# Kernel optimization log

Hardware: AMD Instinct MI355X
Metric: run time of the kernel (lower is better)

The kernel has to match this reference:

```python
import jax, jax.numpy as jnp
import numpy as np

N_NODES = 50000
N_EDGES = 600000
NODE_DIM = 128
EDGE_DIM = 128
HIDDEN = 256
OUT_DIM = 16
MAX_DEG = 10  # PyG MFConv default max_degree
N_GRAPHS = 256
N_MESSAGES = 2


def setup_inputs() -> dict:
    key = jax.random.key(0)
    ks = jax.random.split(key, 10)
    s = 0.05
    x = jax.random.normal(ks[0], (N_NODES, NODE_DIM), jnp.float32)
    edge_attr = jax.random.normal(ks[1], (N_EDGES, EDGE_DIM), jnp.float32)
    edge_index = jax.random.randint(ks[2], (2, N_EDGES), 0, N_NODES, jnp.int32)
    batch = jnp.sort(jax.random.randint(ks[3], (N_NODES,), 0, N_GRAPHS, jnp.int32))
    # MFConv params: lins (on aggregated neighbors, with bias), root_lins (no bias)
    W_lin = jax.random.normal(ks[4], (MAX_DEG + 1, NODE_DIM, NODE_DIM), jnp.float32) * s
    b_lin = jnp.zeros((MAX_DEG + 1, NODE_DIM), jnp.float32)
    W_root = jax.random.normal(ks[5], (MAX_DEG + 1, NODE_DIM, NODE_DIM), jnp.float32) * s
    # EdgeConv nn: Linear(2*edge_dim, edge_dim)
    W_edge = jax.random.normal(ks[6], (2 * EDGE_DIM, EDGE_DIM), jnp.float32) * s
    b_edge = jnp.zeros((EDGE_DIM,), jnp.float32)
    # readout MLP (n_hidden=1): Linear(2*node_dim, hidden), Linear(hidden, out)
    W0 = jax.random.normal(ks[7], (2 * NODE_DIM, HIDDEN), jnp.float32) * s
    b0 = jnp.zeros((HIDDEN,), jnp.float32)
    W1 = jax.random.normal(ks[8], (HIDDEN, OUT_DIM), jnp.float32) * s
    b1 = jnp.zeros((OUT_DIM,), jnp.float32)
    return {"x": x, "edge_attr": edge_attr, "edge_index": edge_index, "batch": batch,
            "W_lin": W_lin, "b_lin": b_lin, "W_root": W_root,
            "W_edge": W_edge, "b_edge": b_edge,
            "W0": W0, "b0": b0, "W1": W1, "b1": b1}


def _mfconv(x, row, col, deg, W_lin, b_lin, W_root):
    # h[i] = sum_{(j->i)} x[j]  (source_to_target flow: row=src, col=dst)
    h = jax.ops.segment_sum(x[row], col, num_segments=N_NODES)
    out = jnp.zeros_like(h)
    for d in range(MAX_DEG + 1):  # fixed small degree-bucket loop
        m = (deg == d).astype(x.dtype)[:, None]
        out = out + m * (h @ W_lin[d] + b_lin[d] + x @ W_root[d])
    return out


def _edgeconv(e, row, col, W, b):
    # message: nn([x_i, x_j - x_i]); aggr = max over incoming edges (empty -> 0)
    xi = e[col]
    msg = jnp.concatenate([xi, e[row] - xi], axis=-1) @ W + b
    out = jax.ops.segment_max(msg, col, num_segments=e.shape[0])
    return jnp.where(jnp.isfinite(out), out, jnp.zeros_like(out))


def reference(x, edge_attr, edge_index, batch, W_lin, b_lin, W_root, W_edge, b_edge, W0, b0, W1, b1):
    row, col = edge_index[0], edge_index[1]
    deg = jnp.clip(jax.ops.segment_sum(jnp.ones((N_EDGES,), jnp.int32), col,
                                       num_segments=N_NODES), 0, MAX_DEG)
    emb_node = x
    emb_edge = edge_attr
    for _ in range(N_MESSAGES):
        x = _mfconv(x, row, col, deg, W_lin, b_lin, W_root)
        emb_node = x
        x = jax.nn.relu(x)  # dropout p=0.0 in eval -> identity
        edge_attr = _edgeconv(edge_attr, row, col, W_edge, b_edge)
        emb_edge = edge_attr
        edge_attr = jax.nn.relu(edge_attr)
    # readout: gather-concat-scatter_add over edges, then global add pool
    out = jnp.concatenate([x[row], edge_attr[col]], axis=-1)  # [E, 2*node_dim]
    out = jax.ops.segment_sum(out, col, num_segments=N_NODES)  # [N, 2*node_dim]
    out = jax.ops.segment_sum(out, batch, num_segments=N_GRAPHS)  # [G, 2*node_dim]
    out = jax.nn.relu(out @ W0 + b0)
    out = jax.nn.relu(out @ W1 + b1)
    return out, emb_node, emb_edge
```

## Files before the change

### kernel.cpp

```cpp
#include <hip/hip_runtime.h>
#include <cfloat>

#define N_NODES 50000
#define N_EDGES 600000
#define DIM 128
#define N_GRAPHS 256
#define HIDDEN 256
#define OUT_DIM 16
#define MAX_DEG 10
#define MAX_TBL 1600
#define GEMM_GRID 1563
#define AGG_GRID 12500
#define EB 2344
#define NB 196
#define XCONV_B 6250
#define WF_B 176
#define WEF_B 16

typedef unsigned short u16;
typedef __attribute__((ext_vector_type(8))) short bf16x8;
typedef __attribute__((ext_vector_type(4))) float f32x4;

__device__ __forceinline__ float bf2f(u16 u) {
  union { unsigned u; float f; } c; c.u = ((unsigned)u) << 16; return c.f;
}
__device__ __forceinline__ u16 f2bf(float f) {
  union { float f; unsigned u; } c; c.f = f;
  return (u16)((c.u + 0x7FFFu + ((c.u >> 16) & 1u)) >> 16);
}
__device__ __forceinline__ float4 relu4(float4 v) {
  return make_float4(fmaxf(v.x, 0.f), fmaxf(v.y, 0.f), fmaxf(v.z, 0.f), fmaxf(v.w, 0.f));
}
__device__ __forceinline__ void fma4b(float4& a, float m, ushort4 v) {
  a.x = fmaf(m, bf2f(v.x), a.x); a.y = fmaf(m, bf2f(v.y), a.y);
  a.z = fmaf(m, bf2f(v.z), a.z); a.w = fmaf(m, bf2f(v.w), a.w);
}
__device__ __forceinline__ void max4b(float4& a, ushort4 v) {
  a.x = fmaxf(a.x, bf2f(v.x)); a.y = fmaxf(a.y, bf2f(v.y));
  a.z = fmaxf(a.z, bf2f(v.z)); a.w = fmaxf(a.w, bf2f(v.w));
}

__global__ __launch_bounds__(256) void kPrep(
    const float* __restrict__ x_in, u16* __restrict__ xb,
    const float* __restrict__ W_lin, const float* __restrict__ W_root,
    u16* __restrict__ Wfrag, const float* __restrict__ W_edge,
    u16* __restrict__ Wefrag, const int* __restrict__ col, int* __restrict__ deg) {
  int b = blockIdx.x, t = threadIdx.x;
  if (b < XCONV_B) {
    size_t i = ((size_t)b * 256 + t) * 4;
    float4 v = *(const float4*)(x_in + i);
    ushort4 o; o.x = f2bf(v.x); o.y = f2bf(v.y); o.z = f2bf(v.z); o.w = f2bf(v.w);
    *(ushort4*)(xb + i) = o;
  } else if (b < XCONV_B + WF_B) {
    int tid = (b - XCONV_B) * 256 + t;
    int lane = tid & 63, f = tid >> 6;
    int d = f >> 6, rem = f & 63, ks = rem >> 3, nt = rem & 7;
    u16* dst = Wfrag + ((size_t)f * 64 + lane) * 8;
    int n = nt * 16 + (lane & 15);
#pragma unroll
    for (int j = 0; j < 8; ++j) {
      int k = ks * 32 + (lane >> 4) * 8 + j;
      float v = (k < 128) ? W_lin[((size_t)d * 128 + k) * 128 + n]
                          : W_root[((size_t)d * 128 + (k - 128)) * 128 + n];
      dst[j] = f2bf(v);
    }
  } else if (b < XCONV_B + WF_B + WEF_B) {
    int tid = (b - XCONV_B - WF_B) * 256 + t;
    int lane = tid & 63, f = tid >> 6;
    int ks = f >> 4, nt = f & 15;
    u16* dst = Wefrag + ((size_t)f * 64 + lane) * 8;
    int n2 = nt * 16 + (lane & 15);
#pragma unroll
    for (int j = 0; j < 8; ++j) {
      int k = ks * 32 + (lane >> 4) * 8 + j;
      float v;
      if (n2 < 128) v = W_edge[(size_t)(128 + k) * 128 + n2];
      else { int n = n2 - 128; v = W_edge[(size_t)k * 128 + n] - W_edge[(size_t)(128 + k) * 128 + n]; }
      dst[j] = f2bf(v);
    }
  } else {
    int e = (b - XCONV_B - WF_B - WEF_B) * 256 + t;
    if (e < N_EDGES) atomicAdd(&deg[col[e]], 1);
  }
}

__global__ void k_setup(const int* __restrict__ deg, const int* __restrict__ batch,
                        int* __restrict__ rowptr, int* __restrict__ cursor,
                        int* __restrict__ bcur, int* __restrict__ tbl_d,
                        int* __restrict__ tbl_base, int* __restrict__ tbl_cnt,
                        int* __restrict__ gstart) {
  __shared__ int tsum[1024];
  __shared__ int hist[MAX_DEG + 1];
  __shared__ int boff[MAX_DEG + 1];
  __shared__ int tblStart[MAX_DEG + 2];
  const int CH = (N_NODES + 1023) / 1024;
  int t = threadIdx.x;
  if (t <= MAX_DEG) hist[t] = 0;
  __syncthreads();
  for (int base2 = 0; base2 < N_NODES; base2 += 1024) {
    int i = base2 + t;
    int d = (i < N_NODES) ? min(deg[i], MAX_DEG) : -1;
#pragma unroll
    for (int dd = 0; dd <= MAX_DEG; ++dd) {
      unsigned long long m = __ballot(d == dd);
      if ((t & 63) == 0 && m) atomicAdd(&hist[dd], (int)__popcll(m));
    }
  }
  int lo = t * CH, hi = min(lo + CH, N_NODES);
  int s = 0;
  for (int i = lo; i < hi; ++i) s += deg[i];
  tsum[t] = s;
  __syncthreads();
  for (int off = 1; off < 1024; off <<= 1) {
    int v = (t >= off) ? tsum[t - off] : 0;
    __syncthreads();
    tsum[t] += v;
    __syncthreads();
  }
  int pre = (t == 0) ? 0 : tsum[t - 1];
  for (int i = lo; i < hi; ++i) { rowptr[i] = pre; cursor[i] = pre; pre += deg[i]; }
  if (t == 1023) rowptr[N_NODES] = tsum[1023];
  if (t == 0) {
    int off = 0, nb = 0;
    for (int d = 0; d <= MAX_DEG; ++d) {
      boff[d] = off; bcur[d] = off; off += hist[d];
      tblStart[d] = nb; nb += (hist[d] + 31) / 32;
    }
    tblStart[MAX_DEG + 1] = nb;
  }
  __syncthreads();
  int totalb = tblStart[MAX_DEG + 1];
  for (int d = 0; d <= MAX_DEG; ++d) {
    int nblk = (hist[d] + 31) / 32;
    int st = tblStart[d];
    for (int idx = t; idx < nblk; idx += 1024) {
      tbl_d[st + idx] = d;
      tbl_base[st + idx] = boff[d] + idx * 32;
      tbl_cnt[st + idx] = min(32, hist[d] - idx * 32);
    }
  }
  for (int idx = totalb + t; idx < MAX_TBL; idx += 1024) tbl_d[idx] = -1;
  for (int g = t; g <= N_GRAPHS; g += 1024) {
    int lo2 = 0, hi2 = N_NODES;
    while (lo2 < hi2) {
      int mid = (lo2 + hi2) >> 1;
      if (batch[mid] < g) lo2 = mid + 1; else hi2 = mid;
    }
    gstart[g] = lo2;
  }
}

template <bool RELUIN, bool F32IN>
__device__ __forceinline__ void dev_EG_mfma(
    int bid, const float* __restrict__ ef, const u16* __restrict__ eb,
    const u16* __restrict__ Wefrag, u16* __restrict__ Bm, float* __restrict__ Cm,
    char* Es ) {
  int base = bid * 32;
  int cnt = min(32, N_NODES - base);
  int tid = threadIdx.x;
  if (F32IN) {
    int i0 = tid >> 5, c4 = (tid & 31) * 4;
#pragma unroll
    for (int it = 0; it < 4; ++it) {
      int i = i0 + it * 8;
      int r = base + min(i, cnt - 1);
      float4 v = *(const float4*)(ef + (size_t)r * DIM + c4);
      if (RELUIN) v = relu4(v);
      ushort4 o; o.x = f2bf(v.x); o.y = f2bf(v.y); o.z = f2bf(v.z); o.w = f2bf(v.w);
      unsigned by = (unsigned)(i * 256 + c4 * 2) ^ (unsigned)((i & 7) << 4);
      *(ushort4*)(Es + by) = o;
    }
  } else {
    int i0 = tid >> 4, c8 = (tid & 15) * 8;
#pragma unroll
    for (int it = 0; it < 2; ++it) {
      int i = i0 + it * 16;
      int r = base + min(i, cnt - 1);
      ushort4 v0 = *(const ushort4*)(eb + (size_t)r * DIM + c8);
      ushort4 v1 = *(const ushort4*)(eb + (size_t)r * DIM + c8 + 4);
      if (RELUIN) {
        v0.x = (v0.x & 0x8000) ? 0 : v0.x; v0.y = (v0.y & 0x8000) ? 0 : v0.y;
        v0.z = (v0.z & 0x8000) ? 0 : v0.z; v0.w = (v0.w & 0x8000) ? 0 : v0.w;
        v1.x = (v1.x & 0x8000) ? 0 : v1.x; v1.y = (v1.y & 0x8000) ? 0 : v1.y;
        v1.z = (v1.z & 0x8000) ? 0 : v1.z; v1.w = (v1.w & 0x8000) ? 0 : v1.w;
      }
      unsigned by = (unsigned)(i * 256 + c8 * 2) ^ (unsigned)((i & 7) << 4);
      *(ushort4*)(Es + by) = v0;
      *(ushort4*)(Es + by + 8) = v1;
    }
  }
  __syncthreads();
  int w = tid >> 6, l = tid & 63, mtile = w & 1, g = w >> 1;
  int l4 = l >> 4, l16 = l & 15;
  f32x4 acc[8];
#pragma unroll
  for (int nt = 0; nt < 8; ++nt) acc[nt] = (f32x4){0.f, 0.f, 0.f, 0.f};
  for (int ks = 0; ks < 4; ++ks) {
    unsigned by = (unsigned)((mtile * 16 + l16) * 256 + ks * 64 + l4 * 16) ^
                  (unsigned)((l16 & 7) << 4);
    bf16x8 af = *(const bf16x8*)(Es + by);
#pragma unroll
    for (int nt = 0; nt < 8; ++nt) {
      int ntile = g * 8 + nt;
      bf16x8 bf = *(const bf16x8*)(Wefrag + (((size_t)ks * 16 + ntile) * 64 + l) * 8);
      acc[nt] = __builtin_amdgcn_mfma_f32_16x16x32_bf16(af, bf, acc[nt], 0, 0, 0);
    }
  }
#pragma unroll
  for (int nt = 0; nt < 8; ++nt) {
    int n2 = (g * 8 + nt) * 16 + l16;
#pragma unroll
    for (int r = 0; r < 4; ++r) {
      int rowi = mtile * 16 + l4 * 4 + r;
      if (rowi < cnt) {
        size_t node = base + rowi;
        if (n2 < 128) Bm[node * DIM + n2] = f2bf(acc[nt][r]);
        else Cm[node * DIM + (n2 - 128)] = acc[nt][r];
      }
    }
  }
}

__global__ __launch_bounds__(256) void k_scatter_fused(
    const int* __restrict__ row, const int* __restrict__ col,
    int* __restrict__ cursor, int* __restrict__ src,
    const int* __restrict__ deg, int* __restrict__ bcur, int* __restrict__ nlist,
    const float* __restrict__ ea, const u16* __restrict__ Wefrag,
    u16* __restrict__ Bm, float* __restrict__ Cm) {
  __shared__ __align__(16) char sm[8192];
  __shared__ int lh[MAX_DEG + 1];
  __shared__ int gbase[MAX_DEG + 1];
  int b = blockIdx.x;
  if (b < NB) {
    int t = threadIdx.x;
    if (t <= MAX_DEG) lh[t] = 0;
    __syncthreads();
    int i = b * 256 + t;
    int bk = 0, r = 0;
    if (i < N_NODES) { bk = min(deg[i], MAX_DEG); r = atomicAdd(&lh[bk], 1); }
    __syncthreads();
    if (t <= MAX_DEG) gbase[t] = lh[t] ? atomicAdd(&bcur[t], lh[t]) : 0;
    __syncthreads();
    if (i < N_NODES) nlist[gbase[bk] + r] = i;
  } else if (b < NB + EB) {
    int e = (b - NB) * 256 + threadIdx.x;
    if (e < N_EDGES) {
      int p = atomicAdd(&cursor[col[e]], 1);
      src[p] = row[e];
    }
  } else {
    dev_EG_mfma<false, true>(b - NB - EB, ea, nullptr, Wefrag, Bm, Cm, sm);
  }
}

template <int MODE>
__device__ __forceinline__ void dev_MF_mfma(
    int b, const u16* __restrict__ xb, const u16* __restrict__ Wfrag,
    const float* __restrict__ b_lin, const int* __restrict__ rowptr,
    const int* __restrict__ src, const int* __restrict__ tbl_d,
    const int* __restrict__ tbl_base, const int* __restrict__ tbl_cnt,
    const int* __restrict__ nlist, float* __restrict__ outf, u16* __restrict__ outb,
    char* As , int* nid) {
  int d = tbl_d[b];
  if (d < 0) return;
  int base = tbl_base[b], cnt = tbl_cnt[b];
  int tid = threadIdx.x;
  if (tid < 32) nid[tid] = nlist[base + min(tid, cnt - 1)];
  __syncthreads();
  int q = tid >> 5, lr = tid & 31;
  for (int i = q; i < 32; i += 8) {
    int node = nid[i];
    int s = rowptr[node], e = rowptr[node + 1], e1 = e - 1;
    float4 a = make_float4(0.f, 0.f, 0.f, 0.f);
    for (int p = s; p < e; p += 8) {
      int idx[8]; float msk[8];
#pragma unroll
      for (int u = 0; u < 8; ++u) {
        int pe = p + u;
        idx[u] = src[min(pe, e1)];
        msk[u] = (pe < e) ? 1.f : 0.f;
      }
#pragma unroll
      for (int u = 0; u < 8; ++u)
        fma4b(a, msk[u], *(const ushort4*)(xb + (size_t)idx[u] * DIM + 4 * lr));
    }
    ushort4 xv = *(const ushort4*)(xb + (size_t)node * DIM + 4 * lr);
    ushort4 hb; hb.x = f2bf(a.x); hb.y = f2bf(a.y); hb.z = f2bf(a.z); hb.w = f2bf(a.w);
    unsigned swz = (unsigned)((i & 7) << 4);
    *(ushort4*)(As + (((unsigned)(i * 512 + 8 * lr)) ^ swz)) = hb;
    *(ushort4*)(As + (((unsigned)(i * 512 + 256 + 8 * lr)) ^ swz)) = xv;
  }
  __syncthreads();
  int w = tid >> 6, l = tid & 63, mtile = w & 1, g = w >> 1;
  int l4 = l >> 4, l16 = l & 15;
  f32x4 acc[4];
#pragma unroll
  for (int nt = 0; nt < 4; ++nt) {
    float bv = b_lin[d * DIM + (g * 4 + nt) * 16 + l16];
    acc[nt] = (f32x4){bv, bv, bv, bv};
  }
  const u16* Wf = Wfrag + (size_t)d * 32768;
  for (int ks = 0; ks < 8; ++ks) {
    unsigned by = (unsigned)((mtile * 16 + l16) * 512 + ks * 64 + l4 * 16) ^
                  (unsigned)((l16 & 7) << 4);
    bf16x8 af = *(const bf16x8*)(As + by);
#pragma unroll
    for (int nt = 0; nt < 4; ++nt) {
      int ntile = g * 4 + nt;
      bf16x8 bf = *(const bf16x8*)(Wf + (((size_t)ks * 8 + ntile) * 64 + l) * 8);
      acc[nt] = __builtin_amdgcn_mfma_f32_16x16x32_bf16(af, bf, acc[nt], 0, 0, 0);
    }
  }
#pragma unroll
  for (int nt = 0; nt < 4; ++nt) {
    int n = (g * 4 + nt) * 16 + l16;
#pragma unroll
    for (int r = 0; r < 4; ++r) {
      int rowi = mtile * 16 + l4 * 4 + r;
      if (rowi < cnt) {
        float v = acc[nt][r];
        size_t o = (size_t)nid[rowi] * DIM + n;
        if (MODE == 1) { outf[o] = v; outb[o] = f2bf(fmaxf(v, 0.f)); }
        else outb[o] = f2bf(fmaxf(v, 0.f));
      }
    }
  }
}

template <bool OUTB, bool WITH_H>
__device__ __forceinline__ void dev_EA(
    int bid, const u16* __restrict__ Bm, const float* __restrict__ Cm,
    const float* __restrict__ b_edge, const int* __restrict__ deg,
    const int* __restrict__ rowptr, const int* __restrict__ src,
    const u16* __restrict__ embNb, u16* __restrict__ outb, float* __restrict__ outf,
    float* __restrict__ h) {
  int w = threadIdx.x >> 6;
  int node = bid * 4 + w;
  if (node >= N_NODES) return;
  int l = threadIdx.x & 63, half = l >> 5, lr = l & 31;
  if (deg[node] == 0) {
    if (half == 0) {
      if (OUTB) {
        ushort4 z; z.x = z.y = z.z = z.w = 0;
        *(ushort4*)(outb + (size_t)node * DIM + 4 * lr) = z;
      } else {
        ((float4*)(outf + (size_t)node * DIM))[lr] = make_float4(0.f, 0.f, 0.f, 0.f);
        if (WITH_H) ((float4*)(h + (size_t)node * DIM))[lr] = make_float4(0.f, 0.f, 0.f, 0.f);
      }
    }
    return;
  }
  int s = rowptr[node], e = rowptr[node + 1], e1 = e - 1;
  float4 m = make_float4(-FLT_MAX, -FLT_MAX, -FLT_MAX, -FLT_MAX);
  float4 a = make_float4(0.f, 0.f, 0.f, 0.f);
  for (int p = s; p < e; p += 8) {
    int idx[4]; float msk[4];
#pragma unroll
    for (int u = 0; u < 4; ++u) {
      int pe = p + 2 * u + half;
      idx[u] = src[min(pe, e1)];
      msk[u] = (pe < e) ? 1.f : 0.f;
    }
#pragma unroll
    for (int u = 0; u < 4; ++u) {
      max4b(m, *(const ushort4*)(Bm + (size_t)idx[u] * DIM + 4 * lr));
      if (WITH_H)
        fma4b(a, msk[u], *(const ushort4*)(embNb + (size_t)idx[u] * DIM + 4 * lr));
    }
  }
  m.x = fmaxf(m.x, __shfl_xor(m.x, 32));
  m.y = fmaxf(m.y, __shfl_xor(m.y, 32));
  m.z = fmaxf(m.z, __shfl_xor(m.z, 32));
  m.w = fmaxf(m.w, __shfl_xor(m.w, 32));
  if (WITH_H) {
    a.x += __shfl_xor(a.x, 32); a.y += __shfl_xor(a.y, 32);
    a.z += __shfl_xor(a.z, 32); a.w += __shfl_xor(a.w, 32);
  }
  if (half == 0) {
    const float4 c = ((const float4*)(Cm + (size_t)node * DIM))[lr];
    const float4 be = ((const float4*)b_edge)[lr];
    float4 o = make_float4(c.x + be.x + m.x, c.y + be.y + m.y,
                           c.z + be.z + m.z, c.w + be.w + m.w);
    if (OUTB) {
      ushort4 ob; ob.x = f2bf(o.x); ob.y = f2bf(o.y); ob.z = f2bf(o.z); ob.w = f2bf(o.w);
      *(ushort4*)(outb + (size_t)node * DIM + 4 * lr) = ob;
    } else {
      ((float4*)(outf + (size_t)node * DIM))[lr] = o;
      if (WITH_H) ((float4*)(h + (size_t)node * DIM))[lr] = a;
    }
  }
}

__global__ __launch_bounds__(256) void kD(
    const u16* __restrict__ xb, const u16* __restrict__ Wfrag,
    const float* __restrict__ b_lin, const int* __restrict__ rowptr,
    const int* __restrict__ src, const int* __restrict__ tbl_d,
    const int* __restrict__ tbl_base, const int* __restrict__ tbl_cnt,
    const int* __restrict__ nlist, u16* __restrict__ tmpNr,
    const u16* __restrict__ Bm, const float* __restrict__ Cm,
    const float* __restrict__ b_edge, const int* __restrict__ deg,
    u16* __restrict__ Em0) {
  __shared__ __align__(16) char sm[16384];
  __shared__ int nid[32];
  if (blockIdx.x < MAX_TBL)
    dev_MF_mfma<0>(blockIdx.x, xb, Wfrag, b_lin, rowptr, src, tbl_d, tbl_base,
                   tbl_cnt, nlist, nullptr, tmpNr, sm, nid);
  else
    dev_EA<true, false>(blockIdx.x - MAX_TBL, Bm, Cm, b_edge, deg, rowptr, src,
                        nullptr, Em0, nullptr, nullptr);
}

__global__ __launch_bounds__(256) void kE(
    const u16* __restrict__ tmpNr, const u16* __restrict__ Wfrag,
    const float* __restrict__ b_lin, const int* __restrict__ rowptr,
    const int* __restrict__ src, const int* __restrict__ tbl_d,
    const int* __restrict__ tbl_base, const int* __restrict__ tbl_cnt,
    const int* __restrict__ nlist, float* __restrict__ embN, u16* __restrict__ embNb,
    const u16* __restrict__ Em0, const u16* __restrict__ Wefrag,
    u16* __restrict__ Bm, float* __restrict__ Cm) {
  __shared__ __align__(16) char sm[16384];
  __shared__ int nid[32];
  if (blockIdx.x < MAX_TBL)
    dev_MF_mfma<1>(blockIdx.x, tmpNr, Wfrag, b_lin, rowptr, src, tbl_d, tbl_base,
                   tbl_cnt, nlist, embN, embNb, sm, nid);
  else
    dev_EG_mfma<true, false>(blockIdx.x - MAX_TBL, nullptr, Em0, Wefrag, Bm, Cm, sm);
}

__global__ __launch_bounds__(256) void kF(
    const u16* __restrict__ Bm, const float* __restrict__ Cm,
    const float* __restrict__ b_edge, const int* __restrict__ deg,
    const int* __restrict__ rowptr, const int* __restrict__ src,
    const u16* __restrict__ embNb, float* __restrict__ embE, float* __restrict__ h) {
  dev_EA<false, true>(blockIdx.x, Bm, Cm, b_edge, deg, rowptr, src, embNb,
                      nullptr, embE, h);
}

__global__ __launch_bounds__(256) void k_readout(
    const float* __restrict__ hf, const float* __restrict__ embE,
    const int* __restrict__ deg, const int* __restrict__ gstart,
    const float* __restrict__ W0, const float* __restrict__ b0,
    const float* __restrict__ W1, const float* __restrict__ b1,
    float* __restrict__ out0) {
  __shared__ float gs[256];
  __shared__ float hid[256];
  int g = blockIdx.x, j = threadIdx.x;
  int s = gstart[g], e = gstart[g + 1];
  float acc = 0.f;
  if (j < DIM) {
    for (int i = s; i < e; ++i) acc += hf[(size_t)i * DIM + j];
  } else {
    int jj = j - DIM;
    for (int i = s; i < e; ++i)
      acc += (float)deg[i] * fmaxf(embE[(size_t)i * DIM + jj], 0.f);
  }
  gs[j] = acc;
  __syncthreads();
  float a0 = b0[j];
  for (int k = 0; k < 256; ++k) a0 += gs[k] * W0[k * 256 + j];
  hid[j] = fmaxf(a0, 0.f);
  __syncthreads();
  if (j < OUT_DIM) {
    float a1 = b1[j];
    for (int k = 0; k < HIDDEN; ++k) a1 += hid[k] * W1[k * OUT_DIM + j];
    out0[g * OUT_DIM + j] = fmaxf(a1, 0.f);
  }
}

extern "C" void kernel_launch(void* const* d_in, const int* in_sizes, int n_in,
                              void* d_out, int out_size, void* d_ws, size_t ws_size,
                              hipStream_t stream) {
  const float* x_in   = (const float*)d_in[0];
  const float* ea_in  = (const float*)d_in[1];
  const int*   ei     = (const int*)d_in[2];
  const int*   batch  = (const int*)d_in[3];
  const float* W_lin  = (const float*)d_in[4];
  const float* b_lin  = (const float*)d_in[5];
  const float* W_root = (const float*)d_in[6];
  const float* W_edge = (const float*)d_in[7];
  const float* b_edge = (const float*)d_in[8];
  const float* W0     = (const float*)d_in[9];
  const float* b0     = (const float*)d_in[10];
  const float* W1     = (const float*)d_in[11];
  const float* b1     = (const float*)d_in[12];
  const int* row = ei;
  const int* col = ei + N_EDGES;

  float* out0 = (float*)d_out;
  float* embN = out0 + N_GRAPHS * OUT_DIM;
  float* embE = embN + (size_t)N_NODES * DIM;

  char* wsp = (char*)d_ws;
  auto alloc = [&](size_t bytes) {
    char* p = wsp;
    wsp += (bytes + 255) & ~(size_t)255;
    return p;
  };
  int* deg      = (int*)alloc((size_t)N_NODES * 4);
  int* rowptr   = (int*)alloc((size_t)(N_NODES + 1) * 4);
  int* cursor   = (int*)alloc((size_t)N_NODES * 4);
  int* src      = (int*)alloc((size_t)N_EDGES * 4);
  int* nlist    = (int*)alloc((size_t)N_NODES * 4);
  int* bcur     = (int*)alloc(16 * 4);
  int* tbl_d    = (int*)alloc(MAX_TBL * 4);
  int* tbl_base = (int*)alloc(MAX_TBL * 4);
  int* tbl_cnt  = (int*)alloc(MAX_TBL * 4);
  int* gstart   = (int*)alloc(257 * 4);
  u16* xb       = (u16*)alloc((size_t)N_NODES * DIM * 2);
  u16* tmpNr    = (u16*)alloc((size_t)N_NODES * DIM * 2);
  u16* embNb    = (u16*)alloc((size_t)N_NODES * DIM * 2);
  u16* Em0      = (u16*)alloc((size_t)N_NODES * DIM * 2);
  u16* Bm       = (u16*)alloc((size_t)N_NODES * DIM * 2);
  float* Cm     = (float*)alloc((size_t)N_NODES * DIM * 4);
  float* h      = (float*)alloc((size_t)N_NODES * DIM * 4);
  u16* Wfrag    = (u16*)alloc((size_t)11 * 8 * 8 * 64 * 8 * 2);
  u16* Wefrag   = (u16*)alloc((size_t)4 * 16 * 64 * 8 * 2);

  hipMemsetAsync(deg, 0, (size_t)N_NODES * 4, stream);
  hipMemsetAsync(embE + (size_t)N_NODES * DIM, 0,
                 (size_t)(N_EDGES - N_NODES) * DIM * sizeof(float), stream);

  kPrep<<<XCONV_B + WF_B + WEF_B + EB, 256, 0, stream>>>(
      x_in, xb, W_lin, W_root, Wfrag, W_edge, Wefrag, col, deg);
  k_setup<<<1, 1024, 0, stream>>>(deg, batch, rowptr, cursor, bcur,
                                  tbl_d, tbl_base, tbl_cnt, gstart);
  k_scatter_fused<<<NB + EB + GEMM_GRID, 256, 0, stream>>>(
      row, col, cursor, src, deg, bcur, nlist, ea_in, Wefrag, Bm, Cm);
  kD<<<MAX_TBL + AGG_GRID, 256, 0, stream>>>(xb, Wfrag, b_lin, rowptr, src,
                                             tbl_d, tbl_base, tbl_cnt, nlist, tmpNr,
                                             Bm, Cm, b_edge, deg, Em0);
  kE<<<MAX_TBL + GEMM_GRID, 256, 0, stream>>>(tmpNr, Wfrag, b_lin, rowptr, src,
                                              tbl_d, tbl_base, tbl_cnt, nlist,
                                              embN, embNb, Em0, Wefrag, Bm, Cm);
  kF<<<AGG_GRID, 256, 0, stream>>>(Bm, Cm, b_edge, deg, rowptr, src, embNb, embE, h);
  k_readout<<<N_GRAPHS, 256, 0, stream>>>(h, embE, deg, gstart, W0, b0, W1, b1, out0);
}
```

Measured before the change: 913.5 us.

## Fuse first edge max-aggregation into MFConv gather, split readout pooling

Folds the first EdgeConv max-aggregation into the MFConv neighbor-gather loop, so both reuse the same CSR indices in one pass. This lets kD drop its separate aggregation blocks and instead zero the embE tail in-kernel, replacing the hipMemsetAsync. Applying ReLU at Em0 write time removes the ReLU-on-input path in the edge GEMM. Readout pooling is split into 8 sub-blocks per graph plus a small MLP kernel to raise parallelism, at the cost of one more launch and a partial-sum buffer.

```diff
diff --git a/kernel.cpp b/kernel.cpp
--- a/kernel.cpp
+++ b/kernel.cpp
@@ -16,6 +16,9 @@
 #define XCONV_B 6250
 #define WF_B 176
 #define WEF_B 16
+#define ZF_B 4096
+#define ZF_N4 17600000
+#define PSUB 8
 
 typedef unsigned short u16;
 typedef __attribute__((ext_vector_type(8))) short bf16x8;
@@ -150,7 +153,7 @@
   }
 }
 
-template <bool RELUIN, bool F32IN>
+template <bool F32IN>
 __device__ __forceinline__ void dev_EG_mfma(
     int bid, const float* __restrict__ ef, const u16* __restrict__ eb,
     const u16* __restrict__ Wefrag, u16* __restrict__ Bm, float* __restrict__ Cm,
@@ -165,7 +168,6 @@
       int i = i0 + it * 8;
       int r = base + min(i, cnt - 1);
       float4 v = *(const float4*)(ef + (size_t)r * DIM + c4);
-      if (RELUIN) v = relu4(v);
       ushort4 o; o.x = f2bf(v.x); o.y = f2bf(v.y); o.z = f2bf(v.z); o.w = f2bf(v.w);
       unsigned by = (unsigned)(i * 256 + c4 * 2) ^ (unsigned)((i & 7) << 4);
       *(ushort4*)(Es + by) = o;
@@ -178,12 +180,6 @@
       int r = base + min(i, cnt - 1);
       ushort4 v0 = *(const ushort4*)(eb + (size_t)r * DIM + c8);
       ushort4 v1 = *(const ushort4*)(eb + (size_t)r * DIM + c8 + 4);
-      if (RELUIN) {
-        v0.x = (v0.x & 0x8000) ? 0 : v0.x; v0.y = (v0.y & 0x8000) ? 0 : v0.y;
-        v0.z = (v0.z & 0x8000) ? 0 : v0.z; v0.w = (v0.w & 0x8000) ? 0 : v0.w;
-        v1.x = (v1.x & 0x8000) ? 0 : v1.x; v1.y = (v1.y & 0x8000) ? 0 : v1.y;
-        v1.z = (v1.z & 0x8000) ? 0 : v1.z; v1.w = (v1.w & 0x8000) ? 0 : v1.w;
-      }
       unsigned by = (unsigned)(i * 256 + c8 * 2) ^ (unsigned)((i & 7) << 4);
       *(ushort4*)(Es + by) = v0;
       *(ushort4*)(Es + by + 8) = v1;
@@ -249,17 +245,19 @@
       src[p] = row[e];
     }
   } else {
-    dev_EG_mfma<false, true>(b - NB - EB, ea, nullptr, Wefrag, Bm, Cm, sm);
-  }
-}
-
-template <int MODE>
+    dev_EG_mfma<true>(b - NB - EB, ea, nullptr, Wefrag, Bm, Cm, sm);
+  }
+}
+
+template <int MODE, bool FUSE_EA>
 __device__ __forceinline__ void dev_MF_mfma(
     int b, const u16* __restrict__ xb, const u16* __restrict__ Wfrag,
     const float* __restrict__ b_lin, const int* __restrict__ rowptr,
     const int* __restrict__ src, const int* __restrict__ tbl_d,
     const int* __restrict__ tbl_base, const int* __restrict__ tbl_cnt,
     const int* __restrict__ nlist, float* __restrict__ outf, u16* __restrict__ outb,
+    const u16* __restrict__ Bm, const float* __restrict__ Cm,
+    const float* __restrict__ b_edge, u16* __restrict__ Em0,
     char* As , int* nid) {
   int d = tbl_d[b];
   if (d < 0) return;
@@ -269,26 +267,45 @@
   __syncthreads();
   int q = tid >> 5, lr = tid & 31;
   for (int i = q; i < 32; i += 8) {
-    int node = nid[i];
-    int s = rowptr[node], e = rowptr[node + 1], e1 = e - 1;
-    float4 a = make_float4(0.f, 0.f, 0.f, 0.f);
-    for (int p = s; p < e; p += 8) {
-      int idx[8]; float msk[8];
-#pragma unroll
-      for (int u = 0; u < 8; ++u) {
-        int pe = p + u;
-        idx[u] = src[min(pe, e1)];
-        msk[u] = (pe < e) ? 1.f : 0.f;
+    if (i < cnt) {
+      int node = nid[i];
+      int s = rowptr[node], e = rowptr[node + 1], e1 = e - 1;
+      float4 a = make_float4(0.f, 0.f, 0.f, 0.f);
+      float4 m = make_float4(-FLT_MAX, -FLT_MAX, -FLT_MAX, -FLT_MAX);
+      for (int p = s; p < e; p += 8) {
+        int idx[8]; float msk[8];
+#pragma unroll
+        for (int u = 0; u < 8; ++u) {
+          int pe = p + u;
+          idx[u] = src[min(pe, e1)];
+          msk[u] = (pe < e) ? 1.f : 0.f;
+        }
+#pragma unroll
+        for (int u = 0; u < 8; ++u) {
+          fma4b(a, msk[u], *(const ushort4*)(xb + (size_t)idx[u] * DIM + 4 * lr));
+          if (FUSE_EA)
+            max4b(m, *(const ushort4*)(Bm + (size_t)idx[u] * DIM + 4 * lr));
+        }
       }
-#pragma unroll
-      for (int u = 0; u < 8; ++u)
-        fma4b(a, msk[u], *(const ushort4*)(xb + (size_t)idx[u] * DIM + 4 * lr));
-    }
-    ushort4 xv = *(const ushort4*)(xb + (size_t)node * DIM + 4 * lr);
-    ushort4 hb; hb.x = f2bf(a.x); hb.y = f2bf(a.y); hb.z = f2bf(a.z); hb.w = f2bf(a.w);
-    unsigned swz = (unsigned)((i & 7) << 4);
-    *(ushort4*)(As + (((unsigned)(i * 512 + 8 * lr)) ^ swz)) = hb;
-    *(ushort4*)(As + (((unsigned)(i * 512 + 256 + 8 * lr)) ^ swz)) = xv;
+      ushort4 xv = *(const ushort4*)(xb + (size_t)node * DIM + 4 * lr);
+      ushort4 hb; hb.x = f2bf(a.x); hb.y = f2bf(a.y); hb.z = f2bf(a.z); hb.w = f2bf(a.w);
+      unsigned swz = (unsigned)((i & 7) << 4);
+      *(ushort4*)(As + (((unsigned)(i * 512 + 8 * lr)) ^ swz)) = hb;
+      *(ushort4*)(As + (((unsigned)(i * 512 + 256 + 8 * lr)) ^ swz)) = xv;
+      if (FUSE_EA) {
+        ushort4 ob;
+        if (s == e) { ob.x = ob.y = ob.z = ob.w = 0; }
+        else {
+          const float4 c = ((const float4*)(Cm + (size_t)node * DIM))[lr];
+          const float4 be = ((const float4*)b_edge)[lr];
+          ob.x = f2bf(fmaxf(c.x + be.x + m.x, 0.f));
+          ob.y = f2bf(fmaxf(c.y + be.y + m.y, 0.f));
+          ob.z = f2bf(fmaxf(c.z + be.z + m.z, 0.f));
+          ob.w = f2bf(fmaxf(c.w + be.w + m.w, 0.f));
+        }
+        *(ushort4*)(Em0 + (size_t)node * DIM + 4 * lr) = ob;
+      }
+    }
   }
   __syncthreads();
   int w = tid >> 6, l = tid & 63, mtile = w & 1, g = w >> 1;
@@ -327,26 +344,19 @@
   }
 }
 
-template <bool OUTB, bool WITH_H>
-__device__ __forceinline__ void dev_EA(
-    int bid, const u16* __restrict__ Bm, const float* __restrict__ Cm,
+__global__ __launch_bounds__(256) void kF(
+    const u16* __restrict__ Bm, const float* __restrict__ Cm,
     const float* __restrict__ b_edge, const int* __restrict__ deg,
     const int* __restrict__ rowptr, const int* __restrict__ src,
-    const u16* __restrict__ embNb, u16* __restrict__ outb, float* __restrict__ outf,
-    float* __restrict__ h) {
+    const u16* __restrict__ embNb, float* __restrict__ embE, float* __restrict__ h) {
   int w = threadIdx.x >> 6;
-  int node = bid * 4 + w;
+  int node = blockIdx.x * 4 + w;
   if (node >= N_NODES) return;
   int l = threadIdx.x & 63, half = l >> 5, lr = l & 31;
   if (deg[node] == 0) {
     if (half == 0) {
-      if (OUTB) {
-        ushort4 z; z.x = z.y = z.z = z.w = 0;
-        *(ushort4*)(outb + (size_t)node * DIM + 4 * lr) = z;
-      } else {
-        ((float4*)(outf + (size_t)node * DIM))[lr] = make_float4(0.f, 0.f, 0.f, 0.f);
-        if (WITH_H) ((float4*)(h + (size_t)node * DIM))[lr] = make_float4(0.f, 0.f, 0.f, 0.f);
-      }
+      ((float4*)(embE + (size_t)node * DIM))[lr] = make_float4(0.f, 0.f, 0.f, 0.f);
+      ((float4*)(h + (size_t)node * DIM))[lr] = make_float4(0.f, 0.f, 0.f, 0.f);
     }
     return;
   }
@@ -364,30 +374,21 @@
 #pragma unroll
     for (int u = 0; u < 4; ++u) {
       max4b(m, *(const ushort4*)(Bm + (size_t)idx[u] * DIM + 4 * lr));
-      if (WITH_H)
-        fma4b(a, msk[u], *(const ushort4*)(embNb + (size_t)idx[u] * DIM + 4 * lr));
+      fma4b(a, msk[u], *(const ushort4*)(embNb + (size_t)idx[u] * DIM + 4 * lr));
     }
   }
   m.x = fmaxf(m.x, __shfl_xor(m.x, 32));
   m.y = fmaxf(m.y, __shfl_xor(m.y, 32));
   m.z = fmaxf(m.z, __shfl_xor(m.z, 32));
   m.w = fmaxf(m.w, __shfl_xor(m.w, 32));
-  if (WITH_H) {
-    a.x += __shfl_xor(a.x, 32); a.y += __shfl_xor(a.y, 32);
-    a.z += __shfl_xor(a.z, 32); a.w += __shfl_xor(a.w, 32);
-  }
+  a.x += __shfl_xor(a.x, 32); a.y += __shfl_xor(a.y, 32);
+  a.z += __shfl_xor(a.z, 32); a.w += __shfl_xor(a.w, 32);
   if (half == 0) {
     const float4 c = ((const float4*)(Cm + (size_t)node * DIM))[lr];
     const float4 be = ((const float4*)b_edge)[lr];
-    float4 o = make_float4(c.x + be.x + m.x, c.y + be.y + m.y,
-                           c.z + be.z + m.z, c.w + be.w + m.w);
-    if (OUTB) {
-      ushort4 ob; ob.x = f2bf(o.x); ob.y = f2bf(o.y); ob.z = f2bf(o.z); ob.w = f2bf(o.w);
-      *(ushort4*)(outb + (size_t)node * DIM + 4 * lr) = ob;
-    } else {
-      ((float4*)(outf + (size_t)node * DIM))[lr] = o;
-      if (WITH_H) ((float4*)(h + (size_t)node * DIM))[lr] = a;
-    }
+    ((float4*)(embE + (size_t)node * DIM))[lr] =
+        make_float4(c.x + be.x + m.x, c.y + be.y + m.y, c.z + be.z + m.z, c.w + be.w + m.w);
+    ((float4*)(h + (size_t)node * DIM))[lr] = a;
   }
 }
 
@@ -398,16 +399,19 @@
     const int* __restrict__ tbl_base, const int* __restrict__ tbl_cnt,
     const int* __restrict__ nlist, u16* __restrict__ tmpNr,
     const u16* __restrict__ Bm, const float* __restrict__ Cm,
-    const float* __restrict__ b_edge, const int* __restrict__ deg,
-    u16* __restrict__ Em0) {
+    const float* __restrict__ b_edge, u16* __restrict__ Em0,
+    float* __restrict__ ztail) {
   __shared__ __align__(16) char sm[16384];
   __shared__ int nid[32];
-  if (blockIdx.x < MAX_TBL)
-    dev_MF_mfma<0>(blockIdx.x, xb, Wfrag, b_lin, rowptr, src, tbl_d, tbl_base,
-                   tbl_cnt, nlist, nullptr, tmpNr, sm, nid);
-  else
-    dev_EA<true, false>(blockIdx.x - MAX_TBL, Bm, Cm, b_edge, deg, rowptr, src,
-                        nullptr, Em0, nullptr, nullptr);
+  if (blockIdx.x < MAX_TBL) {
+    dev_MF_mfma<0, true>(blockIdx.x, xb, Wfrag, b_lin, rowptr, src, tbl_d, tbl_base,
+                         tbl_cnt, nlist, nullptr, tmpNr, Bm, Cm, b_edge, Em0, sm, nid);
+  } else {
+    size_t gid = (size_t)(blockIdx.x - MAX_TBL) * 256 + threadIdx.x;
+    float4 z = make_float4(0.f, 0.f, 0.f, 0.f);
+    for (size_t i = gid; i < ZF_N4; i += (size_t)ZF_B * 256)
+      ((float4*)ztail)[i] = z;
+  }
 }
 
 __global__ __launch_bounds__(256) void kE(
@@ -421,39 +425,44 @@
   __shared__ __align__(16) char sm[16384];
   __shared__ int nid[32];
   if (blockIdx.x < MAX_TBL)
-    dev_MF_mfma<1>(blockIdx.x, tmpNr, Wfrag, b_lin, rowptr, src, tbl_d, tbl_base,
-                   tbl_cnt, nlist, embN, embNb, sm, nid);
+    dev_MF_mfma<1, false>(blockIdx.x, tmpNr, Wfrag, b_lin, rowptr, src, tbl_d, tbl_base,
+                          tbl_cnt, nlist, embN, embNb, nullptr, nullptr, nullptr, nullptr,
+                          sm, nid);
   else
-    dev_EG_mfma<true, false>(blockIdx.x - MAX_TBL, nullptr, Em0, Wefrag, Bm, Cm, sm);
-}
-
-__global__ __launch_bounds__(256) void kF(
-    const u16* __restrict__ Bm, const float* __restrict__ Cm,
-    const float* __restrict__ b_edge, const int* __restrict__ deg,
-    const int* __restrict__ rowptr, const int* __restrict__ src,
-    const u16* __restrict__ embNb, float* __restrict__ embE, float* __restrict__ h) {
-  dev_EA<false, true>(blockIdx.x, Bm, Cm, b_edge, deg, rowptr, src, embNb,
-                      nullptr, embE, h);
-}
-
-__global__ __launch_bounds__(256) void k_readout(
+    dev_EG_mfma<false>(blockIdx.x - MAX_TBL, nullptr, Em0, Wefrag, Bm, Cm, sm);
+}
+
+__global__ __launch_bounds__(256) void kPool(
     const float* __restrict__ hf, const float* __restrict__ embE,
     const int* __restrict__ deg, const int* __restrict__ gstart,
-    const float* __restrict__ W0, const float* __restrict__ b0,
-    const float* __restrict__ W1, const float* __restrict__ b1,
-    float* __restrict__ out0) {
+    float* __restrict__ gfp) {
+  int g = blockIdx.x >> 3, sub = blockIdx.x & (PSUB - 1);
+  int j = threadIdx.x;
+  int s = gstart[g], e = gstart[g + 1];
+  int ch = (e - s + PSUB - 1) / PSUB;
+  int lo = s + sub * ch, hi = min(lo + ch, e);
+  float acc = 0.f;
+  if (j < DIM) {
+    for (int i = lo; i < hi; ++i) acc += hf[(size_t)i * DIM + j];
+  } else {
+    int jj = j - DIM;
+    for (int i = lo; i < hi; ++i)
+      acc += (float)deg[i] * fmaxf(embE[(size_t)i * DIM + jj], 0.f);
+  }
+  gfp[(size_t)blockIdx.x * 256 + j] = acc;
+}
+
+__global__ __launch_bounds__(256) void kMLP(
+    const float* __restrict__ gfp, const float* __restrict__ W0,
+    const float* __restrict__ b0, const float* __restrict__ W1,
+    const float* __restrict__ b1, float* __restrict__ out0) {
   __shared__ float gs[256];
   __shared__ float hid[256];
   int g = blockIdx.x, j = threadIdx.x;
-  int s = gstart[g], e = gstart[g + 1];
   float acc = 0.f;
-  if (j < DIM) {
-    for (int i = s; i < e; ++i) acc += hf[(size_t)i * DIM + j];
-  } else {
-    int jj = j - DIM;
-    for (int i = s; i < e; ++i)
-      acc += (float)deg[i] * fmaxf(embE[(size_t)i * DIM + jj], 0.f);
-  }
+#pragma unroll
+  for (int sub = 0; sub < PSUB; ++sub)
+    acc += gfp[((size_t)g * PSUB + sub) * 256 + j];
   gs[j] = acc;
   __syncthreads();
   float a0 = b0[j];
@@ -513,12 +522,11 @@
   u16* Bm       = (u16*)alloc((size_t)N_NODES * DIM * 2);
   float* Cm     = (float*)alloc((size_t)N_NODES * DIM * 4);
   float* h      = (float*)alloc((size_t)N_NODES * DIM * 4);
+  float* gfp    = (float*)alloc((size_t)N_GRAPHS * PSUB * 256 * 4);
   u16* Wfrag    = (u16*)alloc((size_t)11 * 8 * 8 * 64 * 8 * 2);
   u16* Wefrag   = (u16*)alloc((size_t)4 * 16 * 64 * 8 * 2);
 
   hipMemsetAsync(deg, 0, (size_t)N_NODES * 4, stream);
-  hipMemsetAsync(embE + (size_t)N_NODES * DIM, 0,
-                 (size_t)(N_EDGES - N_NODES) * DIM * sizeof(float), stream);
 
   kPrep<<<XCONV_B + WF_B + WEF_B + EB, 256, 0, stream>>>(
       x_in, xb, W_lin, W_root, Wfrag, W_edge, Wefrag, col, deg);
@@ -526,12 +534,14 @@
                                   tbl_d, tbl_base, tbl_cnt, gstart);
   k_scatter_fused<<<NB + EB + GEMM_GRID, 256, 0, stream>>>(
       row, col, cursor, src, deg, bcur, nlist, ea_in, Wefrag, Bm, Cm);
-  kD<<<MAX_TBL + AGG_GRID, 256, 0, stream>>>(xb, Wfrag, b_lin, rowptr, src,
-                                             tbl_d, tbl_base, tbl_cnt, nlist, tmpNr,
-                                             Bm, Cm, b_edge, deg, Em0);
+  kD<<<MAX_TBL + ZF_B, 256, 0, stream>>>(xb, Wfrag, b_lin, rowptr, src,
+                                         tbl_d, tbl_base, tbl_cnt, nlist, tmpNr,
+                                         Bm, Cm, b_edge, Em0,
+                                         embE + (size_t)N_NODES * DIM);
   kE<<<MAX_TBL + GEMM_GRID, 256, 0, stream>>>(tmpNr, Wfrag, b_lin, rowptr, src,
                                               tbl_d, tbl_base, tbl_cnt, nlist,
                                               embN, embNb, Em0, Wefrag, Bm, Cm);
   kF<<<AGG_GRID, 256, 0, stream>>>(Bm, Cm, b_edge, deg, rowptr, src, embNb, embE, h);
-  k_readout<<<N_GRAPHS, 256, 0, stream>>>(h, embE, deg, gstart, W0, b0, W1, b1, out0);
-}
+  kPool<<<N_GRAPHS * PSUB, 256, 0, stream>>>(h, embE, deg, gstart, gfp);
+  kMLP<<<N_GRAPHS, 256, 0, stream>>>(gfp, W0, b0, W1, b1, out0);
+}
```

Measured after the change: 894.8 us. 1.02x faster.
